# Performance work log

Measured on AMD Instinct MI355X. Metric: run time of the kernel, lower is better.

## Reference

```python
import jax, jax.numpy as jnp
import numpy as np

N_NODES = 8192
N_EDGES = 262144
IN_F, HID, OUT_F = 512, 512, 256


def setup_inputs() -> dict:
    key = jax.random.key(0)
    k_x, k_e, k_w1, k_b1, k_w2, k_b2 = jax.random.split(key, 6)
    x = jax.random.normal(k_x, (N_NODES, IN_F), dtype=jnp.float32)
    edge_index = jax.random.randint(k_e, (2, N_EDGES), 0, N_NODES, dtype=jnp.int64)
    # xavier-uniform linear weights, stored as [in, out]
    def xavier(k, fan_in, fan_out):
        lim = np.sqrt(6.0 / (fan_in + fan_out)).astype(np.float32)
        return jax.random.uniform(k, (fan_in, fan_out), jnp.float32, -lim, lim)
    W1 = xavier(k_w1, IN_F, HID)
    b1 = jax.random.uniform(k_b1, (HID,), jnp.float32, -0.05, 0.05)
    W2 = xavier(k_w2, HID, OUT_F)
    b2 = jax.random.uniform(k_b2, (OUT_F,), jnp.float32, -0.05, 0.05)
    return {"x": x, "edge_index": edge_index, "W1": W1, "b1": b1, "W2": W2, "b2": b2}


def _gcn_layer(x, edge_index, W, b):
    # H' = D~^{-1/2} A~ D~^{-1/2} H W + b, with A~ = A + I
    n = x.shape[0]
    adj = jnp.zeros((n, n), dtype=x.dtype).at[edge_index[0], edge_index[1]].set(1.0)
    adj = adj + jnp.eye(n, dtype=x.dtype)
    degree = jnp.clip(adj.sum(axis=1), 1.0, None)
    d_inv_sqrt = degree ** -0.5
    adj_norm = adj * d_inv_sqrt[None, :] * d_inv_sqrt[:, None]
    return (adj_norm @ x) @ W + b


def reference(x, edge_index, W1, b1, W2, b2):
    h = jax.nn.relu(_gcn_layer(x, edge_index, W1, b1))
    # dropout p=0.0 -> identity
    out = _gcn_layer(h, edge_index, W2, b2)
    return out
```

## Files before the change

### kernel.cpp

```cpp
#include <hip/hip_runtime.h>
#include <hip/hip_bf16.h>
#include <stdint.h>

#define N_NODES 8192
#define N_EDGES 262144
#define IN_F 512
#define HID 512
#define OUT_F 256
#define CAP 128

typedef __attribute__((ext_vector_type(8))) short short8;
typedef __attribute__((ext_vector_type(4))) float f32x4;

__device__ __forceinline__ float bflo(unsigned int u) {
  union { unsigned int x; float f; } c; c.x = u << 16; return c.f;
}
__device__ __forceinline__ float bfhi(unsigned int u) {
  union { unsigned int x; float f; } c; c.x = u & 0xffff0000u; return c.f;
}
__device__ __forceinline__ unsigned short f2bf(float f) {
  union { float f; unsigned int u; } c; c.f = f;
  unsigned int r = c.u + 0x7fffu + ((c.u >> 16) & 1u);
  return (unsigned short)(r >> 16);
}

__device__ __forceinline__ void gload_lds16(const void* g, void* l) {
  __builtin_amdgcn_global_load_lds((const __attribute__((address_space(1))) void*)g,
                                   (__attribute__((address_space(3))) void*)l, 16, 0, 0);
}

__global__ void build_adj(const int* __restrict__ ei, unsigned int* __restrict__ bitmap,
                          int* __restrict__ cnt, int* __restrict__ adj) {
  int e = blockIdx.x * blockDim.x + threadIdx.x;
  if (e >= N_EDGES) return;
  int i = ei[e];
  int j = ei[N_EDGES + e];
  int lin = i * N_NODES + j;
  unsigned int bit = 1u << (lin & 31);
  unsigned int old = atomicOr(&bitmap[lin >> 5], bit);
  if (!(old & bit)) {
    int p = atomicAdd(&cnt[i], 1);
    if (p < CAP) adj[i * CAP + p] = j;
  }
}

__global__ void calc_dis(const int* __restrict__ cnt, float* __restrict__ dis) {
  int i = blockIdx.x * blockDim.x + threadIdx.x;
  if (i < N_NODES) dis[i] = rsqrtf((float)(cnt[i] + 1));
}

__global__ void cvt_bf16_vec(const float* __restrict__ in, unsigned short* __restrict__ out, int n4) {
  int idx = blockIdx.x * blockDim.x + threadIdx.x;
  if (idx >= n4) return;
  const float4 v = ((const float4*)in)[idx];
  uint2 o;
  o.x = (unsigned int)f2bf(v.x) | ((unsigned int)f2bf(v.y) << 16);
  o.y = (unsigned int)f2bf(v.z) | ((unsigned int)f2bf(v.w) << 16);
  ((uint2*)out)[idx] = o;
}

__global__ void transpose_bf16(const float* __restrict__ W, unsigned short* __restrict__ Wt,
                               int K, int N) {
  int idx = blockIdx.x * blockDim.x + threadIdx.x;
  if (idx >= K * N) return;
  int k = idx / N, n = idx - k * N;
  Wt[n * K + k] = f2bf(W[idx]);
}

__global__ __launch_bounds__(256) void gemm_bt(
    const unsigned short* __restrict__ A, const unsigned short* __restrict__ Bt,
    unsigned short* __restrict__ C, int M, int N, int K) {
  __shared__ __align__(16) unsigned short As[128 * 64];
  __shared__ __align__(16) unsigned short Bs[128 * 64];
  const int tid = threadIdx.x;
  const long row0 = (long)blockIdx.x * 128;
  const long col0 = (long)blockIdx.y * 128;
  const int lane = tid & 63;
  const int wid = tid >> 6;
  const int ln15 = lane & 15, hi = lane >> 4;
  const int wr = (wid >> 1) * 64, wc = (wid & 1) * 64;
  const int sr = tid >> 3;
  const int sk = (tid & 7) * 8;
  f32x4 acc[4][4] = {};

  for (int k0 = 0; k0 < K; k0 += 64) {
#pragma unroll
    for (int c = 0; c < 4; ++c) {
      gload_lds16(A  + (row0 + c * 32 + sr) * (long)K + k0 + sk, &As[(c * 256 + tid) * 8]);
      gload_lds16(Bt + (col0 + c * 32 + sr) * (long)K + k0 + sk, &Bs[(c * 256 + tid) * 8]);
    }
    __syncthreads();
#pragma unroll
    for (int kk = 0; kk < 64; kk += 32) {
      short8 a[4], b[4];
#pragma unroll
      for (int m = 0; m < 4; ++m)
        a[m] = *(const short8*)&As[(wr + m * 16 + ln15) * 64 + kk + hi * 8];
#pragma unroll
      for (int n = 0; n < 4; ++n)
        b[n] = *(const short8*)&Bs[(wc + n * 16 + ln15) * 64 + kk + hi * 8];
#pragma unroll
      for (int m = 0; m < 4; ++m)
#pragma unroll
        for (int n = 0; n < 4; ++n)
          acc[m][n] = __builtin_amdgcn_mfma_f32_16x16x32_bf16(a[m], b[n], acc[m][n], 0, 0, 0);
    }
    __syncthreads();
  }
#pragma unroll
  for (int m = 0; m < 4; ++m)
#pragma unroll
    for (int n = 0; n < 4; ++n) {
#pragma unroll
      for (int r = 0; r < 4; ++r) {
        long row = row0 + wr + m * 16 + hi * 4 + r;
        long col = col0 + wc + n * 16 + ln15;
        C[row * N + col] = f2bf(acc[m][n][r]);
      }
    }
}

__global__ __launch_bounds__(256) void aggregate_relu(
    const unsigned short* __restrict__ T, const int* __restrict__ cnt,
    const int* __restrict__ adj, const float* __restrict__ dis,
    const float* __restrict__ bias, unsigned short* __restrict__ H) {
  const int i = blockIdx.x;
  const int t = threadIdx.x;
  __shared__ int js[CAP];
  __shared__ float ws[CAP];
  int n = cnt[i]; if (n > CAP) n = CAP;
  if (t < CAP && t < n) { int j = adj[i * CAP + t]; js[t] = j; ws[t] = dis[j]; }
  __syncthreads();
  const float di = dis[i];
  unsigned int u = *(const unsigned int*)&T[(long)i * 512 + t * 2];
  float a0 = di * bflo(u), a1 = di * bfhi(u);
  for (int e = 0; e < n; ++e) {
    unsigned int v = *(const unsigned int*)&T[(long)js[e] * 512 + t * 2];
    float w = ws[e];
    a0 += w * bflo(v); a1 += w * bfhi(v);
  }
  float h0 = fmaxf(di * a0 + bias[t * 2], 0.f);
  float h1 = fmaxf(di * a1 + bias[t * 2 + 1], 0.f);
  unsigned int o = (unsigned int)f2bf(h0) | ((unsigned int)f2bf(h1) << 16);
  *(unsigned int*)&H[(long)i * 512 + t * 2] = o;
}

__global__ __launch_bounds__(128) void aggregate_out(
    const unsigned short* __restrict__ T, const int* __restrict__ cnt,
    const int* __restrict__ adj, const float* __restrict__ dis,
    const float* __restrict__ bias, float* __restrict__ out) {
  const int i = blockIdx.x;
  const int t = threadIdx.x;
  __shared__ int js[CAP];
  __shared__ float ws[CAP];
  int n = cnt[i]; if (n > CAP) n = CAP;
  if (t < n) { int j = adj[i * CAP + t]; js[t] = j; ws[t] = dis[j]; }
  __syncthreads();
  const float di = dis[i];
  unsigned int u = *(const unsigned int*)&T[(long)i * 256 + t * 2];
  float a0 = di * bflo(u), a1 = di * bfhi(u);
  for (int e = 0; e < n; ++e) {
    unsigned int v = *(const unsigned int*)&T[(long)js[e] * 256 + t * 2];
    float w = ws[e];
    a0 += w * bflo(v); a1 += w * bfhi(v);
  }
  float2 o;
  o.x = di * a0 + bias[t * 2];
  o.y = di * a1 + bias[t * 2 + 1];
  *(float2*)&out[(long)i * 256 + t * 2] = o;
}

extern "C" void kernel_launch(void* const* d_in, const int* in_sizes, int n_in,
                              void* d_out, int out_size, void* d_ws, size_t ws_size,
                              hipStream_t stream) {
  const float* x  = (const float*)d_in[0];
  const int*   ei = (const int*)d_in[1];
  const float* W1 = (const float*)d_in[2];
  const float* b1 = (const float*)d_in[3];
  const float* W2 = (const float*)d_in[4];
  const float* b2 = (const float*)d_in[5];
  float* out = (float*)d_out;

  char* ws = (char*)d_ws;
  unsigned int* bitmap = (unsigned int*)ws;  ws += 8388608;
  int* cnt   = (int*)ws;                     ws += 32768;
  int* adj   = (int*)ws;                     ws += (size_t)N_NODES * CAP * 4;
  float* dis = (float*)ws;                   ws += 32768;
  unsigned short* Xb  = (unsigned short*)ws; ws += (size_t)N_NODES * IN_F * 2;
  unsigned short* W1t = (unsigned short*)ws; ws += (size_t)IN_F * HID * 2;
  unsigned short* W2t = (unsigned short*)ws; ws += (size_t)HID * OUT_F * 2;
  unsigned short* T1  = (unsigned short*)ws; ws += (size_t)N_NODES * HID * 2;
  unsigned short* H   = (unsigned short*)ws; ws += (size_t)N_NODES * HID * 2;
  unsigned short* T2  = (unsigned short*)ws; ws += (size_t)N_NODES * OUT_F * 2;

  hipMemsetAsync(bitmap, 0, 8388608 + 32768, stream);

  build_adj<<<N_EDGES / 256, 256, 0, stream>>>(ei, bitmap, cnt, adj);
  calc_dis<<<N_NODES / 256, 256, 0, stream>>>(cnt, dis);

  cvt_bf16_vec<<<(N_NODES * IN_F / 4 + 255) / 256, 256, 0, stream>>>(x, Xb, N_NODES * IN_F / 4);
  transpose_bf16<<<(IN_F * HID + 255) / 256, 256, 0, stream>>>(W1, W1t, IN_F, HID);
  transpose_bf16<<<(HID * OUT_F + 255) / 256, 256, 0, stream>>>(W2, W2t, HID, OUT_F);

  gemm_bt<<<dim3(64, 4), 256, 0, stream>>>(Xb, W1t, T1, N_NODES, HID, IN_F);
  aggregate_relu<<<N_NODES, 256, 0, stream>>>(T1, cnt, adj, dis, b1, H);

  gemm_bt<<<dim3(64, 2), 256, 0, stream>>>(H, W2t, T2, N_NODES, OUT_F, HID);
  aggregate_out<<<N_NODES, 128, 0, stream>>>(T2, cnt, adj, dis, b2, out);
}
```

Measured before the change: 180.4 us.

## Split neighbor aggregation across waves, smaller GEMM tiles, fuse prep kernels

The aggregation kernels now give each wave a strided subset of neighbors, with 16-byte (or 8-byte) row loads per lane. Per-wave partial sums are reduced through shared memory, and the inverse-sqrt degree is computed inline, so the calc_dis kernel goes away. The GEMM is templated and launched with smaller tiles (128x64 and 64x64) to put more blocks on the GPU. The two weight-transpose launches are merged into one kernel. The changes target launch count, the serial per-thread neighbor loop, and low GEMM grid occupancy, at the cost of an extra LDS reduction and more redundant loads from smaller tiles.

```diff
diff --git a/kernel.cpp b/kernel.cpp
--- a/kernel.cpp
+++ b/kernel.cpp
@@ -29,8 +29,9 @@
                                    (__attribute__((address_space(3))) void*)l, 16, 0, 0);
 }
 
-__global__ void build_adj(const int* __restrict__ ei, unsigned int* __restrict__ bitmap,
-                          int* __restrict__ cnt, int* __restrict__ adj) {
+__global__ __launch_bounds__(256) void build_adj(
+    const int* __restrict__ ei, unsigned int* __restrict__ bitmap,
+    int* __restrict__ cnt, int* __restrict__ adj) {
   int e = blockIdx.x * blockDim.x + threadIdx.x;
   if (e >= N_EDGES) return;
   int i = ei[e];
@@ -44,12 +45,8 @@
   }
 }
 
-__global__ void calc_dis(const int* __restrict__ cnt, float* __restrict__ dis) {
-  int i = blockIdx.x * blockDim.x + threadIdx.x;
-  if (i < N_NODES) dis[i] = rsqrtf((float)(cnt[i] + 1));
-}
-
-__global__ void cvt_bf16_vec(const float* __restrict__ in, unsigned short* __restrict__ out, int n4) {
+__global__ __launch_bounds__(256) void cvt_bf16_vec(
+    const float* __restrict__ in, unsigned short* __restrict__ out, int n4) {
   int idx = blockIdx.x * blockDim.x + threadIdx.x;
   if (idx >= n4) return;
   const float4 v = ((const float4*)in)[idx];
@@ -59,115 +56,139 @@
   ((uint2*)out)[idx] = o;
 }
 
-__global__ void transpose_bf16(const float* __restrict__ W, unsigned short* __restrict__ Wt,
-                               int K, int N) {
+__global__ __launch_bounds__(256) void prep_weights(
+    const float* __restrict__ W1, const float* __restrict__ W2,
+    unsigned short* __restrict__ W1t, unsigned short* __restrict__ W2t) {
   int idx = blockIdx.x * blockDim.x + threadIdx.x;
-  if (idx >= K * N) return;
-  int k = idx / N, n = idx - k * N;
-  Wt[n * K + k] = f2bf(W[idx]);
-}
-
+  if (idx < IN_F * HID) {
+    int k = idx >> 9, n = idx & 511;
+    W1t[n * IN_F + k] = f2bf(W1[idx]);
+  } else {
+    int r = idx - IN_F * HID;
+    if (r < HID * OUT_F) {
+      int k = r >> 8, n = r & 255;
+      W2t[n * HID + k] = f2bf(W2[r]);
+    }
+  }
+}
+
+template<int BM, int BN>
 __global__ __launch_bounds__(256) void gemm_bt(
     const unsigned short* __restrict__ A, const unsigned short* __restrict__ Bt,
     unsigned short* __restrict__ C, int M, int N, int K) {
-  __shared__ __align__(16) unsigned short As[128 * 64];
-  __shared__ __align__(16) unsigned short Bs[128 * 64];
+  constexpr int MR = BM / 32, NR = BN / 32;
+  __shared__ __align__(16) unsigned short As[BM * 64];
+  __shared__ __align__(16) unsigned short Bs[BN * 64];
   const int tid = threadIdx.x;
-  const long row0 = (long)blockIdx.x * 128;
-  const long col0 = (long)blockIdx.y * 128;
+  const long row0 = (long)blockIdx.x * BM;
+  const long col0 = (long)blockIdx.y * BN;
   const int lane = tid & 63;
   const int wid = tid >> 6;
   const int ln15 = lane & 15, hi = lane >> 4;
-  const int wr = (wid >> 1) * 64, wc = (wid & 1) * 64;
+  const int wr = (wid >> 1) * (BM / 2), wc = (wid & 1) * (BN / 2);
   const int sr = tid >> 3;
   const int sk = (tid & 7) * 8;
-  f32x4 acc[4][4] = {};
+  f32x4 acc[MR][NR] = {};
 
   for (int k0 = 0; k0 < K; k0 += 64) {
 #pragma unroll
-    for (int c = 0; c < 4; ++c) {
+    for (int c = 0; c < MR; ++c)
       gload_lds16(A  + (row0 + c * 32 + sr) * (long)K + k0 + sk, &As[(c * 256 + tid) * 8]);
+#pragma unroll
+    for (int c = 0; c < NR; ++c)
       gload_lds16(Bt + (col0 + c * 32 + sr) * (long)K + k0 + sk, &Bs[(c * 256 + tid) * 8]);
-    }
     __syncthreads();
 #pragma unroll
     for (int kk = 0; kk < 64; kk += 32) {
-      short8 a[4], b[4];
-#pragma unroll
-      for (int m = 0; m < 4; ++m)
+      short8 a[MR], b[NR];
+#pragma unroll
+      for (int m = 0; m < MR; ++m)
         a[m] = *(const short8*)&As[(wr + m * 16 + ln15) * 64 + kk + hi * 8];
 #pragma unroll
-      for (int n = 0; n < 4; ++n)
+      for (int n = 0; n < NR; ++n)
         b[n] = *(const short8*)&Bs[(wc + n * 16 + ln15) * 64 + kk + hi * 8];
 #pragma unroll
-      for (int m = 0; m < 4; ++m)
-#pragma unroll
-        for (int n = 0; n < 4; ++n)
+      for (int m = 0; m < MR; ++m)
+#pragma unroll
+        for (int n = 0; n < NR; ++n)
           acc[m][n] = __builtin_amdgcn_mfma_f32_16x16x32_bf16(a[m], b[n], acc[m][n], 0, 0, 0);
     }
     __syncthreads();
   }
 #pragma unroll
-  for (int m = 0; m < 4; ++m)
-#pragma unroll
-    for (int n = 0; n < 4; ++n) {
+  for (int m = 0; m < MR; ++m)
+#pragma unroll
+    for (int n = 0; n < NR; ++n)
 #pragma unroll
       for (int r = 0; r < 4; ++r) {
         long row = row0 + wr + m * 16 + hi * 4 + r;
         long col = col0 + wc + n * 16 + ln15;
         C[row * N + col] = f2bf(acc[m][n][r]);
       }
-    }
 }
 
 __global__ __launch_bounds__(256) void aggregate_relu(
     const unsigned short* __restrict__ T, const int* __restrict__ cnt,
-    const int* __restrict__ adj, const float* __restrict__ dis,
-    const float* __restrict__ bias, unsigned short* __restrict__ H) {
+    const int* __restrict__ adj, const float* __restrict__ bias,
+    unsigned short* __restrict__ H) {
   const int i = blockIdx.x;
-  const int t = threadIdx.x;
+  const int tid = threadIdx.x;
+  const int lane = tid & 63, w = tid >> 6;
   __shared__ int js[CAP];
   __shared__ float ws[CAP];
+  __shared__ float part[4][512];
   int n = cnt[i]; if (n > CAP) n = CAP;
-  if (t < CAP && t < n) { int j = adj[i * CAP + t]; js[t] = j; ws[t] = dis[j]; }
-  __syncthreads();
-  const float di = dis[i];
-  unsigned int u = *(const unsigned int*)&T[(long)i * 512 + t * 2];
-  float a0 = di * bflo(u), a1 = di * bfhi(u);
-  for (int e = 0; e < n; ++e) {
-    unsigned int v = *(const unsigned int*)&T[(long)js[e] * 512 + t * 2];
-    float w = ws[e];
-    a0 += w * bflo(v); a1 += w * bfhi(v);
-  }
-  float h0 = fmaxf(di * a0 + bias[t * 2], 0.f);
-  float h1 = fmaxf(di * a1 + bias[t * 2 + 1], 0.f);
-  unsigned int o = (unsigned int)f2bf(h0) | ((unsigned int)f2bf(h1) << 16);
-  *(unsigned int*)&H[(long)i * 512 + t * 2] = o;
-}
-
-__global__ __launch_bounds__(128) void aggregate_out(
+  if (tid < n) { int j = adj[i * CAP + tid]; js[tid] = j; ws[tid] = rsqrtf((float)(cnt[j] + 1)); }
+  __syncthreads();
+  float a[8] = {};
+  for (int e = w; e < n; e += 4) {
+    const uint4 v = *(const uint4*)&T[(long)js[e] * 512 + lane * 8];
+    float wj = ws[e];
+    a[0] += wj * bflo(v.x); a[1] += wj * bfhi(v.x);
+    a[2] += wj * bflo(v.y); a[3] += wj * bfhi(v.y);
+    a[4] += wj * bflo(v.z); a[5] += wj * bfhi(v.z);
+    a[6] += wj * bflo(v.w); a[7] += wj * bfhi(v.w);
+  }
+  *(float4*)&part[w][lane * 8]     = make_float4(a[0], a[1], a[2], a[3]);
+  *(float4*)&part[w][lane * 8 + 4] = make_float4(a[4], a[5], a[6], a[7]);
+  __syncthreads();
+  const float di = rsqrtf((float)(cnt[i] + 1));
+  unsigned int u = *(const unsigned int*)&T[(long)i * 512 + tid * 2];
+  float s0 = part[0][2*tid]   + part[1][2*tid]   + part[2][2*tid]   + part[3][2*tid]   + di * bflo(u);
+  float s1 = part[0][2*tid+1] + part[1][2*tid+1] + part[2][2*tid+1] + part[3][2*tid+1] + di * bfhi(u);
+  const float2 bb = *(const float2*)&bias[2 * tid];
+  float h0 = fmaxf(di * s0 + bb.x, 0.f);
+  float h1 = fmaxf(di * s1 + bb.y, 0.f);
+  *(unsigned int*)&H[(long)i * 512 + tid * 2] =
+      (unsigned int)f2bf(h0) | ((unsigned int)f2bf(h1) << 16);
+}
+
+__global__ __launch_bounds__(256) void aggregate_out(
     const unsigned short* __restrict__ T, const int* __restrict__ cnt,
-    const int* __restrict__ adj, const float* __restrict__ dis,
-    const float* __restrict__ bias, float* __restrict__ out) {
+    const int* __restrict__ adj, const float* __restrict__ bias,
+    float* __restrict__ out) {
   const int i = blockIdx.x;
-  const int t = threadIdx.x;
+  const int tid = threadIdx.x;
+  const int lane = tid & 63, w = tid >> 6;
   __shared__ int js[CAP];
   __shared__ float ws[CAP];
+  __shared__ float part[4][256];
   int n = cnt[i]; if (n > CAP) n = CAP;
-  if (t < n) { int j = adj[i * CAP + t]; js[t] = j; ws[t] = dis[j]; }
-  __syncthreads();
-  const float di = dis[i];
-  unsigned int u = *(const unsigned int*)&T[(long)i * 256 + t * 2];
-  float a0 = di * bflo(u), a1 = di * bfhi(u);
-  for (int e = 0; e < n; ++e) {
-    unsigned int v = *(const unsigned int*)&T[(long)js[e] * 256 + t * 2];
-    float w = ws[e];
-    a0 += w * bflo(v); a1 += w * bfhi(v);
-  }
-  float2 o;
-  o.x = di * a0 + bias[t * 2];
-  o.y = di * a1 + bias[t * 2 + 1];
-  *(float2*)&out[(long)i * 256 + t * 2] = o;
+  if (tid < n) { int j = adj[i * CAP + tid]; js[tid] = j; ws[tid] = rsqrtf((float)(cnt[j] + 1)); }
+  __syncthreads();
+  float a[4] = {};
+  for (int e = w; e < n; e += 4) {
+    const uint2 v = *(const uint2*)&T[(long)js[e] * 256 + lane * 4];
+    float wj = ws[e];
+    a[0] += wj * bflo(v.x); a[1] += wj * bfhi(v.x);
+    a[2] += wj * bflo(v.y); a[3] += wj * bfhi(v.y);
+  }
+  *(float4*)&part[w][lane * 4] = make_float4(a[0], a[1], a[2], a[3]);
+  __syncthreads();
+  const float di = rsqrtf((float)(cnt[i] + 1));
+  float self = di * __uint_as_float(((unsigned int)T[(long)i * 256 + tid]) << 16);
+  float s = part[0][tid] + part[1][tid] + part[2][tid] + part[3][tid] + self;
+  out[(long)i * 256 + tid] = di * s + bias[tid];
 }
 
 extern "C" void kernel_launch(void* const* d_in, const int* in_sizes, int n_in,
@@ -185,7 +206,6 @@
   unsigned int* bitmap = (unsigned int*)ws;  ws += 8388608;
   int* cnt   = (int*)ws;                     ws += 32768;
   int* adj   = (int*)ws;                     ws += (size_t)N_NODES * CAP * 4;
-  float* dis = (float*)ws;                   ws += 32768;
   unsigned short* Xb  = (unsigned short*)ws; ws += (size_t)N_NODES * IN_F * 2;
   unsigned short* W1t = (unsigned short*)ws; ws += (size_t)IN_F * HID * 2;
   unsigned short* W2t = (unsigned short*)ws; ws += (size_t)HID * OUT_F * 2;
@@ -196,15 +216,13 @@
   hipMemsetAsync(bitmap, 0, 8388608 + 32768, stream);
 
   build_adj<<<N_EDGES / 256, 256, 0, stream>>>(ei, bitmap, cnt, adj);
-  calc_dis<<<N_NODES / 256, 256, 0, stream>>>(cnt, dis);
-
-  cvt_bf16_vec<<<(N_NODES * IN_F / 4 + 255) / 256, 256, 0, stream>>>(x, Xb, N_NODES * IN_F / 4);
-  transpose_bf16<<<(IN_F * HID + 255) / 256, 256, 0, stream>>>(W1, W1t, IN_F, HID);
-  transpose_bf16<<<(HID * OUT_F + 255) / 256, 256, 0, stream>>>(W2, W2t, HID, OUT_F);
-
-  gemm_bt<<<dim3(64, 4), 256, 0, stream>>>(Xb, W1t, T1, N_NODES, HID, IN_F);
-  aggregate_relu<<<N_NODES, 256, 0, stream>>>(T1, cnt, adj, dis, b1, H);
-
-  gemm_bt<<<dim3(64, 2), 256, 0, stream>>>(H, W2t, T2, N_NODES, OUT_F, HID);
-  aggregate_out<<<N_NODES, 128, 0, stream>>>(T2, cnt, adj, dis, b2, out);
-}
+
+  cvt_bf16_vec<<<N_NODES * IN_F / 4 / 256, 256, 0, stream>>>(x, Xb, N_NODES * IN_F / 4);
+  prep_weights<<<(IN_F * HID + HID * OUT_F) / 256, 256, 0, stream>>>(W1, W2, W1t, W2t);
+
+  gemm_bt<128, 64><<<dim3(N_NODES / 128, HID / 64), 256, 0, stream>>>(Xb, W1t, T1, N_NODES, HID, IN_F);
+  aggregate_relu<<<N_NODES, 256, 0, stream>>>(T1, cnt, adj, b1, H);
+
+  gemm_bt<64, 64><<<dim3(N_NODES / 64, OUT_F / 64), 256, 0, stream>>>(H, W2t, T2, N_NODES, OUT_F, HID);
+  aggregate_out<<<N_NODES, 256, 0, stream>>>(T2, cnt, adj, b2, out);
+}
```

Measured after the change: 175.1 us. -3.0%, faster.
